# Optimization experiments

Measured on AMD Instinct MI355X. Metric: run time of the kernel, lower is better.

The kernel has to match this reference:

```python
import jax, jax.numpy as jnp
import numpy as np

CODE_DIM = 256
CODEBOOK_SIZE = 8192
N = 32768
BETA = 0.25


def setup_inputs() -> dict:
    key = jax.random.key(0)
    k1, k2 = jax.random.split(key)
    z = jax.random.normal(k1, (N, CODE_DIM), dtype=jnp.float32)
    # nn.Embedding weight init: uniform(-1/code_dim, 1/code_dim)
    codebook = jax.random.uniform(
        k2, (CODEBOOK_SIZE, CODE_DIM), dtype=jnp.float32,
        minval=-1.0 / CODE_DIM, maxval=1.0 / CODE_DIM)
    return {"z": z, "codebook": codebook}


def reference(z, codebook):
    # z: (N, D) already flat (z.view(N, -1) in torch). codebook: (K, D)
    # squared euclidean distances via expansion: ||z||^2 - 2 z.E^T + ||E||^2
    z_sq = jnp.sum(z * z, axis=1, keepdims=True)            # (N, 1)
    e_sq = jnp.sum(codebook * codebook, axis=1)             # (K,)
    dist = z_sq - 2.0 * (z @ codebook.T) + e_sq[None, :]    # (N, K)
    indices = jnp.argmin(dist, axis=1)                      # (N,)
    z_q = codebook[indices]                                 # (N, D)

    commitment_loss = jnp.mean((jax.lax.stop_gradient(z_q) - z) ** 2)
    codebook_loss = jnp.mean((z_q - jax.lax.stop_gradient(z)) ** 2)
    loss = BETA * commitment_loss + codebook_loss

    # straight-through estimator
    z_q_ste = z + jax.lax.stop_gradient(z_q - z)
    return (z_q_ste, loss)
```

## Files before the change

kernel.cpp:

```cpp
#include <hip/hip_runtime.h>
#include <cfloat>

#define NROWS  32768
#define NCODES 8192
#define DDIM   256
#define KG     4
#define CPB    (NCODES / KG)
#define CT     32
#define TPB    (CPB / CT)
#define RPB    128

typedef __attribute__((ext_vector_type(8)))  __bf16 bf16x8;
typedef __attribute__((ext_vector_type(16))) float  f32x16;

__global__ __launch_bounds__(256)
void cvt_cb(const float* __restrict__ cb, __bf16* __restrict__ cbb,
            float* __restrict__ esq) {
    const size_t i = (size_t)(blockIdx.x * 256 + threadIdx.x) * 8;
    const float4 f0 = *(const float4*)(cb + i);
    const float4 f1 = *(const float4*)(cb + i + 4);
    bf16x8 v;
    v[0] = (__bf16)f0.x; v[1] = (__bf16)f0.y; v[2] = (__bf16)f0.z; v[3] = (__bf16)f0.w;
    v[4] = (__bf16)f1.x; v[5] = (__bf16)f1.y; v[6] = (__bf16)f1.z; v[7] = (__bf16)f1.w;
    *(bf16x8*)(cbb + i) = v;
    float s = f0.x * f0.x + f0.y * f0.y + f0.z * f0.z + f0.w * f0.w
            + f1.x * f1.x + f1.y * f1.y + f1.z * f1.z + f1.w * f1.w;
    for (int o = 16; o > 0; o >>= 1) s += __shfl_down(s, o, 32);
    if ((threadIdx.x & 31) == 0) esq[i >> 8] = s + 1.0f;
}

__global__ __launch_bounds__(128, 2)
void vq_mfma(const float* __restrict__ z, const __bf16* __restrict__ cbb,
             const float* __restrict__ esq, unsigned* __restrict__ pK) {
    __shared__ __align__(16) __bf16 Bb[2][CT * DDIM];

    const int rowbase  = (blockIdx.x >> 2) * RPB;
    const int kg       = blockIdx.x & 3;
    const int codebase = kg * CPB;

    const int tid = threadIdx.x;
    const int w = tid >> 6, l = tid & 63;
    const int la = l & 31, lh = l >> 5;
    const int loff = la * DDIM + lh * 8;

#pragma unroll
    for (int jj = 0; jj < 8; ++jj) {
        const int p = w * 8 + jj;
        __builtin_amdgcn_global_load_lds(
            (const __attribute__((address_space(1))) void*)
                (cbb + (size_t)codebase * DDIM + p * 16 + loff),
            (__attribute__((address_space(3))) void*)(&Bb[0][p * 512]),
            16, 0, 0);
    }

    bf16x8 Af[2][16];
    {
        const float* zp = z + (size_t)(rowbase + w * 64 + la) * DDIM + lh * 8;
#pragma unroll
        for (int s = 0; s < 2; ++s)
#pragma unroll
            for (int kc = 0; kc < 16; ++kc) {
                const float4 f0 = *(const float4*)(zp + s * 32 * DDIM + kc * 16);
                const float4 f1 = *(const float4*)(zp + s * 32 * DDIM + kc * 16 + 4);
                bf16x8 v;
                v[0] = (__bf16)(-2.f * f0.x); v[1] = (__bf16)(-2.f * f0.y);
                v[2] = (__bf16)(-2.f * f0.z); v[3] = (__bf16)(-2.f * f0.w);
                v[4] = (__bf16)(-2.f * f1.x); v[5] = (__bf16)(-2.f * f1.y);
                v[6] = (__bf16)(-2.f * f1.z); v[7] = (__bf16)(-2.f * f1.w);
                Af[s][kc] = v;
            }
    }

    float evc, evn;
    evc = esq[codebase + la];

    unsigned bestK[32];
#pragma unroll
    for (int s = 0; s < 32; ++s) bestK[s] = 0xFFFFFFFFu;

    __syncthreads();

    int buf = 0;
#pragma unroll 1
    for (int t = 0; t < TPB; ++t) {
        if (t + 1 < TPB) {
            const __bf16* base = cbb + (size_t)(codebase + (t + 1) * CT) * DDIM;
#pragma unroll
            for (int jj = 0; jj < 8; ++jj) {
                const int p = w * 8 + jj;
                __builtin_amdgcn_global_load_lds(
                    (const __attribute__((address_space(1))) void*)
                        (base + p * 16 + loff),
                    (__attribute__((address_space(3))) void*)(&Bb[buf ^ 1][p * 512]),
                    16, 0, 0);
            }
        }
        {
            const int tn = (t + 1) & (TPB - 1);
            evn = esq[codebase + tn * CT + la];
        }

        const __bf16* Bc = &Bb[buf][0];

        f32x16 acc0, acc1;
#pragma unroll
        for (int r = 0; r < 16; ++r) { acc0[r] = evc; acc1[r] = evc; }
        __builtin_amdgcn_s_setprio(1);
#pragma unroll
        for (int kc = 0; kc < 16; ++kc) {
            const bf16x8 b = *(const bf16x8*)(Bc + kc * 512 + l * 8);
            acc0 = __builtin_amdgcn_mfma_f32_32x32x16_bf16(Af[0][kc], b, acc0, 0, 0, 0);
            acc1 = __builtin_amdgcn_mfma_f32_32x32x16_bf16(Af[1][kc], b, acc1, 0, 0, 0);
        }
        __builtin_amdgcn_s_setprio(0);
        {
            const unsigned cA = (unsigned)(codebase + t * CT + la);
#pragma unroll
            for (int r = 0; r < 16; ++r) {
                const unsigned k0 = (__float_as_uint(acc0[r]) & 0xFFFFE000u) | cA;
                if (k0 < bestK[r])      bestK[r]      = k0;
                const unsigned k1 = (__float_as_uint(acc1[r]) & 0xFFFFE000u) | cA;
                if (k1 < bestK[16 + r]) bestK[16 + r] = k1;
            }
        }

        evc = evn;

        __syncthreads();
        buf ^= 1;
    }

#pragma unroll
    for (int s = 0; s < 32; ++s) {
#pragma unroll
        for (int m = 1; m < 32; m <<= 1) {
            const unsigned k2 = (unsigned)__shfl_xor((int)bestK[s], m);
            if (k2 < bestK[s]) bestK[s] = k2;
        }
    }
    if (la == 0) {
#pragma unroll
        for (int s = 0; s < 2; ++s)
#pragma unroll
            for (int r = 0; r < 16; ++r) {
                const int rl = w * 64 + s * 32 + (r & 3) + 8 * (r >> 2) + 4 * lh;
                pK[(size_t)(rowbase + rl) * KG + kg] = bestK[s * 16 + r];
            }
    }
}

__global__ __launch_bounds__(256)
void vq_finalize(const float* __restrict__ z, const float* __restrict__ cb,
                 const unsigned* __restrict__ pK,
                 float* __restrict__ out, float* __restrict__ bsum) {
    __shared__ float sSum[4];
    __shared__ int   sIdx[4];
    const int tid = threadIdx.x;
    const int rw = tid >> 6, lane = tid & 63;
    const int row = blockIdx.x * 4 + rw;

    if (lane == 0) {
        unsigned k = pK[row * KG];
#pragma unroll
        for (int q = 1; q < KG; ++q) {
            const unsigned k2 = pK[row * KG + q];
            if (k2 < k) k = k2;
        }
        sIdx[rw] = (int)(k & 0x1FFFu);
    }
    __syncthreads();
    const int idx = sIdx[rw];

    const float4 zv = *(const float4*)(z  + (size_t)row * DDIM + lane * 4);
    const float4 ev = *(const float4*)(cb + (size_t)idx * DDIM + lane * 4);
    float4 d, o;
    d.x = ev.x - zv.x; d.y = ev.y - zv.y; d.z = ev.z - zv.z; d.w = ev.w - zv.w;
    o.x = zv.x + d.x;  o.y = zv.y + d.y;  o.z = zv.z + d.z;  o.w = zv.w + d.w;
    *(float4*)(out + (size_t)row * DDIM + lane * 4) = o;

    float s = d.x * d.x + d.y * d.y + d.z * d.z + d.w * d.w;
    for (int off = 32; off > 0; off >>= 1) s += __shfl_down(s, off);
    if (lane == 0) sSum[rw] = s;
    __syncthreads();
    if (tid == 0) bsum[blockIdx.x] = sSum[0] + sSum[1] + sSum[2] + sSum[3];
}

__global__ __launch_bounds__(256)
void loss_final(const float* __restrict__ bsum, float* __restrict__ out) {
    __shared__ float red[4];
    const int tid = threadIdx.x;
    float s = 0.f;
    for (int i = tid; i < NROWS / 4; i += 256) s += bsum[i];
    for (int off = 32; off > 0; off >>= 1) s += __shfl_down(s, off);
    const int wv = tid >> 6, lane = tid & 63;
    if (lane == 0) red[wv] = s;
    __syncthreads();
    if (tid == 0) {
        const float tot = red[0] + red[1] + red[2] + red[3];
        out[(size_t)NROWS * DDIM] = tot * (1.25f / (float)((size_t)NROWS * DDIM));
    }
}

extern "C" void kernel_launch(void* const* d_in, const int* in_sizes, int n_in,
                              void* d_out, int out_size, void* d_ws, size_t ws_size,
                              hipStream_t stream) {
    const float* z  = (const float*)d_in[0];
    const float* cb = (const float*)d_in[1];
    float* out = (float*)d_out;

    __bf16* cbf = (__bf16*)d_out;

    float*    esq  = (float*)d_ws;
    unsigned* pK   = (unsigned*)(esq + NCODES);
    float*    bsum = (float*)(pK + NROWS * KG);

    cvt_cb<<<NCODES * DDIM / 8 / 256, 256, 0, stream>>>(cb, cbf, esq);
    vq_mfma<<<(NROWS / RPB) * KG, 128, 0, stream>>>(z, cbf, esq, pK);
    vq_finalize<<<NROWS / 4, 256, 0, stream>>>(z, cb, pK, out, bsum);
    loss_final<<<1, 256, 0, stream>>>(bsum, out);
}
```

Measured before the change: 251.1 us.

## Use per-wave codebook buffers with 16x16 MFMA and drop block barriers

Moves the distance GEMM from 32x32x16 to 16x16x32 bf16 MFMA and doubles rows per block to 256 across four waves. Each wave now streams its own double-buffered codebook tile into private LDS and waits on vmcnt, so the per-iteration __syncthreads is gone. Codebook norms are staged once in LDS instead of being loaded from global every iteration. The cost is that each wave fetches its own copy of the codebook tiles, which roughly doubles codebook read traffic per row-code pair.

```diff
diff --git a/kernel.cpp b/kernel.cpp
--- a/kernel.cpp
+++ b/kernel.cpp
@@ -6,12 +6,12 @@
 #define DDIM   256
 #define KG     4
 #define CPB    (NCODES / KG)
-#define CT     32
-#define TPB    (CPB / CT)
-#define RPB    128
-
-typedef __attribute__((ext_vector_type(8)))  __bf16 bf16x8;
-typedef __attribute__((ext_vector_type(16))) float  f32x16;
+#define CW     16
+#define TPB    (CPB / CW)
+#define RPB    256
+
+typedef __attribute__((ext_vector_type(8))) __bf16 bf16x8;
+typedef __attribute__((ext_vector_type(4))) float  f32x4;
 
 __global__ __launch_bounds__(256)
 void cvt_cb(const float* __restrict__ cb, __bf16* __restrict__ cbb,
@@ -29,10 +29,11 @@
     if ((threadIdx.x & 31) == 0) esq[i >> 8] = s + 1.0f;
 }
 
-__global__ __launch_bounds__(128, 2)
+__global__ __launch_bounds__(256, 2)
 void vq_mfma(const float* __restrict__ z, const __bf16* __restrict__ cbb,
              const float* __restrict__ esq, unsigned* __restrict__ pK) {
-    __shared__ __align__(16) __bf16 Bb[2][CT * DDIM];
+    __shared__ __align__(16) __bf16 Bw[4][2][CW * DDIM];
+    __shared__ __align__(16) float  esqLds[CPB];
 
     const int rowbase  = (blockIdx.x >> 2) * RPB;
     const int kg       = blockIdx.x & 3;
@@ -40,28 +41,34 @@
 
     const int tid = threadIdx.x;
     const int w = tid >> 6, l = tid & 63;
-    const int la = l & 31, lh = l >> 5;
-    const int loff = la * DDIM + lh * 8;
-
-#pragma unroll
-    for (int jj = 0; jj < 8; ++jj) {
-        const int p = w * 8 + jj;
+    const int lm = l & 15, lq = l >> 4;
+    const int loff = lm * DDIM + lq * 8;
+
+#pragma unroll
+    for (int j = 0; j < 8; ++j) {
         __builtin_amdgcn_global_load_lds(
             (const __attribute__((address_space(1))) void*)
-                (cbb + (size_t)codebase * DDIM + p * 16 + loff),
-            (__attribute__((address_space(3))) void*)(&Bb[0][p * 512]),
+                (cbb + (size_t)codebase * DDIM + j * 32 + loff),
+            (__attribute__((address_space(3))) void*)(&Bw[w][0][j * 512]),
             16, 0, 0);
     }
 
-    bf16x8 Af[2][16];
     {
-        const float* zp = z + (size_t)(rowbase + w * 64 + la) * DDIM + lh * 8;
-#pragma unroll
-        for (int s = 0; s < 2; ++s)
-#pragma unroll
-            for (int kc = 0; kc < 16; ++kc) {
-                const float4 f0 = *(const float4*)(zp + s * 32 * DDIM + kc * 16);
-                const float4 f1 = *(const float4*)(zp + s * 32 * DDIM + kc * 16 + 4);
+        const float4 q0 = *(const float4*)(esq + codebase + tid * 8);
+        const float4 q1 = *(const float4*)(esq + codebase + tid * 8 + 4);
+        *(float4*)&esqLds[tid * 8]     = q0;
+        *(float4*)&esqLds[tid * 8 + 4] = q1;
+    }
+
+    bf16x8 Af[4][8];
+    {
+        const float* zp = z + (size_t)(rowbase + w * 64 + lm) * DDIM + lq * 8;
+#pragma unroll
+        for (int s = 0; s < 4; ++s)
+#pragma unroll
+            for (int kc = 0; kc < 8; ++kc) {
+                const float4 f0 = *(const float4*)(zp + s * 16 * DDIM + kc * 32);
+                const float4 f1 = *(const float4*)(zp + s * 16 * DDIM + kc * 32 + 4);
                 bf16x8 v;
                 v[0] = (__bf16)(-2.f * f0.x); v[1] = (__bf16)(-2.f * f0.y);
                 v[2] = (__bf16)(-2.f * f0.z); v[3] = (__bf16)(-2.f * f0.w);
@@ -71,12 +78,9 @@
             }
     }
 
-    float evc, evn;
-    evc = esq[codebase + la];
-
-    unsigned bestK[32];
-#pragma unroll
-    for (int s = 0; s < 32; ++s) bestK[s] = 0xFFFFFFFFu;
+    unsigned bestK[16];
+#pragma unroll
+    for (int s = 0; s < 16; ++s) bestK[s] = 0xFFFFFFFFu;
 
     __syncthreads();
 
@@ -84,68 +88,65 @@
 #pragma unroll 1
     for (int t = 0; t < TPB; ++t) {
         if (t + 1 < TPB) {
-            const __bf16* base = cbb + (size_t)(codebase + (t + 1) * CT) * DDIM;
-#pragma unroll
-            for (int jj = 0; jj < 8; ++jj) {
-                const int p = w * 8 + jj;
+            const __bf16* src = cbb + (size_t)(codebase + (t + 1) * CW) * DDIM;
+#pragma unroll
+            for (int j = 0; j < 8; ++j) {
                 __builtin_amdgcn_global_load_lds(
-                    (const __attribute__((address_space(1))) void*)
-                        (base + p * 16 + loff),
-                    (__attribute__((address_space(3))) void*)(&Bb[buf ^ 1][p * 512]),
+                    (const __attribute__((address_space(1))) void*)(src + j * 32 + loff),
+                    (__attribute__((address_space(3))) void*)(&Bw[w][buf ^ 1][j * 512]),
                     16, 0, 0);
             }
-        }
+            asm volatile("s_waitcnt vmcnt(8)" ::: "memory");
+        } else {
+            asm volatile("s_waitcnt vmcnt(0)" ::: "memory");
+        }
+
+        const float e = esqLds[t * CW + lm];
+        f32x4 acc[4];
+#pragma unroll
+        for (int s = 0; s < 4; ++s) acc[s] = (f32x4){e, e, e, e};
+
+        const __bf16* Bc = &Bw[w][buf][0];
+        __builtin_amdgcn_s_setprio(1);
+#pragma unroll
+        for (int kc = 0; kc < 8; ++kc) {
+            const bf16x8 b = *(const bf16x8*)(Bc + kc * 512 + l * 8);
+#pragma unroll
+            for (int s = 0; s < 4; ++s)
+                acc[s] = __builtin_amdgcn_mfma_f32_16x16x32_bf16(
+                    Af[s][kc], b, acc[s], 0, 0, 0);
+        }
+        __builtin_amdgcn_s_setprio(0);
+
         {
-            const int tn = (t + 1) & (TPB - 1);
-            evn = esq[codebase + tn * CT + la];
-        }
-
-        const __bf16* Bc = &Bb[buf][0];
-
-        f32x16 acc0, acc1;
-#pragma unroll
-        for (int r = 0; r < 16; ++r) { acc0[r] = evc; acc1[r] = evc; }
-        __builtin_amdgcn_s_setprio(1);
-#pragma unroll
-        for (int kc = 0; kc < 16; ++kc) {
-            const bf16x8 b = *(const bf16x8*)(Bc + kc * 512 + l * 8);
-            acc0 = __builtin_amdgcn_mfma_f32_32x32x16_bf16(Af[0][kc], b, acc0, 0, 0, 0);
-            acc1 = __builtin_amdgcn_mfma_f32_32x32x16_bf16(Af[1][kc], b, acc1, 0, 0, 0);
-        }
-        __builtin_amdgcn_s_setprio(0);
-        {
-            const unsigned cA = (unsigned)(codebase + t * CT + la);
-#pragma unroll
-            for (int r = 0; r < 16; ++r) {
-                const unsigned k0 = (__float_as_uint(acc0[r]) & 0xFFFFE000u) | cA;
-                if (k0 < bestK[r])      bestK[r]      = k0;
-                const unsigned k1 = (__float_as_uint(acc1[r]) & 0xFFFFE000u) | cA;
-                if (k1 < bestK[16 + r]) bestK[16 + r] = k1;
-            }
-        }
-
-        evc = evn;
-
-        __syncthreads();
+            const unsigned cI = (unsigned)(codebase + t * CW + lm);
+#pragma unroll
+            for (int s = 0; s < 4; ++s)
+#pragma unroll
+                for (int i = 0; i < 4; ++i) {
+                    const unsigned k = (__float_as_uint(acc[s][i]) & 0xFFFFE000u) | cI;
+                    const int slot = s * 4 + i;
+                    if (k < bestK[slot]) bestK[slot] = k;
+                }
+        }
+
         buf ^= 1;
     }
 
 #pragma unroll
-    for (int s = 0; s < 32; ++s) {
-#pragma unroll
-        for (int m = 1; m < 32; m <<= 1) {
+    for (int s = 0; s < 16; ++s) {
+#pragma unroll
+        for (int m = 1; m < 16; m <<= 1) {
             const unsigned k2 = (unsigned)__shfl_xor((int)bestK[s], m);
             if (k2 < bestK[s]) bestK[s] = k2;
         }
     }
-    if (la == 0) {
-#pragma unroll
-        for (int s = 0; s < 2; ++s)
-#pragma unroll
-            for (int r = 0; r < 16; ++r) {
-                const int rl = w * 64 + s * 32 + (r & 3) + 8 * (r >> 2) + 4 * lh;
-                pK[(size_t)(rowbase + rl) * KG + kg] = bestK[s * 16 + r];
-            }
+    if (lm == 0) {
+#pragma unroll
+        for (int s = 0; s < 16; ++s) {
+            const int rl = w * 64 + (s >> 2) * 16 + lq * 4 + (s & 3);
+            pK[(size_t)(rowbase + rl) * KG + kg] = bestK[s];
+        }
     }
 }
 
@@ -215,7 +216,7 @@
     float*    bsum = (float*)(pK + NROWS * KG);
 
     cvt_cb<<<NCODES * DDIM / 8 / 256, 256, 0, stream>>>(cb, cbf, esq);
-    vq_mfma<<<(NROWS / RPB) * KG, 128, 0, stream>>>(z, cbf, esq, pK);
+    vq_mfma<<<(NROWS / RPB) * KG, 256, 0, stream>>>(z, cbf, esq, pK);
     vq_finalize<<<NROWS / 4, 256, 0, stream>>>(z, cb, pK, out, bsum);
     loss_final<<<1, 256, 0, stream>>>(bsum, out);
 }
```

After: 352.9 us. +40.6%, slower.

## Use 256-thread blocks with triple-buffered codebook tiles and LDS-staged code norms

Applied to the files above, without the earlier changes.

Doubles rows per block to 256 with four waves, so each codebook tile loaded into LDS is reused by twice as many rows and global codebook traffic halves. Codebook staging moves from double to triple buffering with a prefetch distance of two tiles and explicit vmcnt waits plus a raw barrier instead of __syncthreads. Code norms are preloaded into LDS once and folded into the first MFMA as the initial accumulator. In exchange, LDS per block grows and occupancy may fall, and the hand-written waitcnt counts must match the number of outstanding loads.

```diff
diff --git a/kernel.cpp b/kernel.cpp
--- a/kernel.cpp
+++ b/kernel.cpp
@@ -8,7 +8,7 @@
 #define CPB    (NCODES / KG)
 #define CT     32
 #define TPB    (CPB / CT)
-#define RPB    128
+#define RPB    256
 
 typedef __attribute__((ext_vector_type(8)))  __bf16 bf16x8;
 typedef __attribute__((ext_vector_type(16))) float  f32x16;
@@ -29,10 +29,11 @@
     if ((threadIdx.x & 31) == 0) esq[i >> 8] = s + 1.0f;
 }
 
-__global__ __launch_bounds__(128, 2)
+__global__ __launch_bounds__(256, 2)
 void vq_mfma(const float* __restrict__ z, const __bf16* __restrict__ cbb,
              const float* __restrict__ esq, unsigned* __restrict__ pK) {
-    __shared__ __align__(16) __bf16 Bb[2][CT * DDIM];
+    __shared__ __align__(16) __bf16 Bb[3][CT * DDIM];
+    __shared__ __align__(16) float  esqLds[CPB];
 
     const int rowbase  = (blockIdx.x >> 2) * RPB;
     const int kg       = blockIdx.x & 3;
@@ -42,15 +43,26 @@
     const int w = tid >> 6, l = tid & 63;
     const int la = l & 31, lh = l >> 5;
     const int loff = la * DDIM + lh * 8;
-
-#pragma unroll
-    for (int jj = 0; jj < 8; ++jj) {
-        const int p = w * 8 + jj;
-        __builtin_amdgcn_global_load_lds(
-            (const __attribute__((address_space(1))) void*)
-                (cbb + (size_t)codebase * DDIM + p * 16 + loff),
-            (__attribute__((address_space(3))) void*)(&Bb[0][p * 512]),
-            16, 0, 0);
+    const int kcb = w * 4;
+
+#pragma unroll
+    for (int s0 = 0; s0 < 2; ++s0) {
+        const __bf16* src = cbb + (size_t)(codebase + s0 * CT) * DDIM;
+#pragma unroll
+        for (int jj = 0; jj < 4; ++jj) {
+            const int kc = kcb + jj;
+            __builtin_amdgcn_global_load_lds(
+                (const __attribute__((address_space(1))) void*)(src + kc * 16 + loff),
+                (__attribute__((address_space(3))) void*)(&Bb[s0][kc * 512]),
+                16, 0, 0);
+        }
+    }
+
+    {
+        const float4 q0 = *(const float4*)(esq + codebase + tid * 8);
+        const float4 q1 = *(const float4*)(esq + codebase + tid * 8 + 4);
+        *(float4*)&esqLds[tid * 8]     = q0;
+        *(float4*)&esqLds[tid * 8 + 4] = q1;
     }
 
     bf16x8 Af[2][16];
@@ -71,63 +83,67 @@
             }
     }
 
-    float evc, evn;
-    evc = esq[codebase + la];
-
     unsigned bestK[32];
 #pragma unroll
     for (int s = 0; s < 32; ++s) bestK[s] = 0xFFFFFFFFu;
 
-    __syncthreads();
-
-    int buf = 0;
+    asm volatile("s_waitcnt vmcnt(0) lgkmcnt(0)" ::: "memory");
+    __builtin_amdgcn_s_barrier();
+
+    int sc = 0;
 #pragma unroll 1
     for (int t = 0; t < TPB; ++t) {
-        if (t + 1 < TPB) {
-            const __bf16* base = cbb + (size_t)(codebase + (t + 1) * CT) * DDIM;
-#pragma unroll
-            for (int jj = 0; jj < 8; ++jj) {
-                const int p = w * 8 + jj;
+        if (t + 2 < TPB) {
+            int sp = sc + 2; if (sp >= 3) sp -= 3;
+            const __bf16* src = cbb + (size_t)(codebase + (t + 2) * CT) * DDIM;
+#pragma unroll
+            for (int jj = 0; jj < 4; ++jj) {
+                const int kc = kcb + jj;
                 __builtin_amdgcn_global_load_lds(
-                    (const __attribute__((address_space(1))) void*)
-                        (base + p * 16 + loff),
-                    (__attribute__((address_space(3))) void*)(&Bb[buf ^ 1][p * 512]),
+                    (const __attribute__((address_space(1))) void*)(src + kc * 16 + loff),
+                    (__attribute__((address_space(3))) void*)(&Bb[sp][kc * 512]),
                     16, 0, 0);
             }
         }
+
+        const float e = esqLds[t * CT + la];
+        f32x16 einit;
+#pragma unroll
+        for (int r = 0; r < 16; ++r) einit[r] = e;
+        const __bf16* Bc = &Bb[sc][0];
+        f32x16 acc0, acc1;
+        __builtin_amdgcn_s_setprio(1);
         {
-            const int tn = (t + 1) & (TPB - 1);
-            evn = esq[codebase + tn * CT + la];
-        }
-
-        const __bf16* Bc = &Bb[buf][0];
-
-        f32x16 acc0, acc1;
-#pragma unroll
-        for (int r = 0; r < 16; ++r) { acc0[r] = evc; acc1[r] = evc; }
-        __builtin_amdgcn_s_setprio(1);
-#pragma unroll
-        for (int kc = 0; kc < 16; ++kc) {
+            const bf16x8 b = *(const bf16x8*)(Bc + l * 8);
+            acc0 = __builtin_amdgcn_mfma_f32_32x32x16_bf16(Af[0][0], b, einit, 0, 0, 0);
+            acc1 = __builtin_amdgcn_mfma_f32_32x32x16_bf16(Af[1][0], b, einit, 0, 0, 0);
+        }
+#pragma unroll
+        for (int kc = 1; kc < 16; ++kc) {
             const bf16x8 b = *(const bf16x8*)(Bc + kc * 512 + l * 8);
             acc0 = __builtin_amdgcn_mfma_f32_32x32x16_bf16(Af[0][kc], b, acc0, 0, 0, 0);
             acc1 = __builtin_amdgcn_mfma_f32_32x32x16_bf16(Af[1][kc], b, acc1, 0, 0, 0);
         }
         __builtin_amdgcn_s_setprio(0);
+
+        if (t + 2 < TPB)
+            asm volatile("s_waitcnt vmcnt(4) lgkmcnt(0)" ::: "memory");
+        else
+            asm volatile("s_waitcnt vmcnt(0) lgkmcnt(0)" ::: "memory");
+        __builtin_amdgcn_s_barrier();
+
         {
-            const unsigned cA = (unsigned)(codebase + t * CT + la);
+            const unsigned cI = (unsigned)(codebase + t * CT + la);
 #pragma unroll
             for (int r = 0; r < 16; ++r) {
-                const unsigned k0 = (__float_as_uint(acc0[r]) & 0xFFFFE000u) | cA;
+                const unsigned k0 = (__float_as_uint(acc0[r]) & 0xFFFFE000u) | cI;
                 if (k0 < bestK[r])      bestK[r]      = k0;
-                const unsigned k1 = (__float_as_uint(acc1[r]) & 0xFFFFE000u) | cA;
+                const unsigned k1 = (__float_as_uint(acc1[r]) & 0xFFFFE000u) | cI;
                 if (k1 < bestK[16 + r]) bestK[16 + r] = k1;
             }
         }
 
-        evc = evn;
-
-        __syncthreads();
-        buf ^= 1;
+        ++sc; if (sc >= 3) sc -= 3;
     }
 
 #pragma unroll
@@ -215,7 +231,7 @@
     float*    bsum = (float*)(pK + NROWS * KG);
 
     cvt_cb<<<NCODES * DDIM / 8 / 256, 256, 0, stream>>>(cb, cbf, esq);
-    vq_mfma<<<(NROWS / RPB) * KG, 128, 0, stream>>>(z, cbf, esq, pK);
+    vq_mfma<<<(NROWS / RPB) * KG, 256, 0, stream>>>(z, cbf, esq, pK);
     vq_finalize<<<NROWS / 4, 256, 0, stream>>>(z, cb, pK, out, bsum);
     loss_final<<<1, 256, 0, stream>>>(bsum, out);
 }
```

Result: faster. 241.3 us (-3.9%).
